# Kernel optimization log

Measured on AMD Instinct MI355X. Metric: run time of the kernel, lower is better.

Reference implementation:

```python
import jax, jax.numpy as jnp
import numpy as np

B, N, C, H = 8, 1024, 512, 8
DH = C // H
SCALE = DH ** -0.5
NEG = -1.0e9


def setup_inputs() -> dict:
    key = jax.random.key(0)
    ks = jax.random.split(key, 8)
    s = lambda fan: 1.0 / np.sqrt(fan)
    return {
        "x": jax.random.normal(ks[0], (B, N, C), jnp.float32),
        "mask": jnp.ones((B, N), jnp.float32),
        "qkv_w": jax.random.normal(ks[1], (3 * C, C), jnp.float32) * s(C),
        "qkv_b": jnp.zeros((3 * C,), jnp.float32),
        "proj_w_mat": jax.random.normal(ks[2], (C, C), jnp.float32) * s(C),
        "proj_b": jnp.zeros((C,), jnp.float32),
        "pl_w": jax.random.normal(ks[3], (H, H), jnp.float32) * s(H),
        "pl_b": jnp.zeros((H,), jnp.float32),
        "pw_w": jax.random.normal(ks[4], (H, H), jnp.float32) * s(H),
        "pw_b": jnp.zeros((H,), jnp.float32),
    }


def reference(x, mask, qkv_w, qkv_b, proj_w_mat, proj_b, pl_w, pl_b, pw_w, pw_b):
    b, n, c = x.shape
    h = pl_w.shape[0]
    dh = c // h
    # qkv: [B,N,3C] -> [3,B,H,N,Dh]
    qkv = (x @ qkv_w.T + qkv_b).reshape(b, n, 3, h, dh).transpose(2, 0, 3, 1, 4)
    q, k, v = qkv[0] * SCALE, qkv[1], qkv[2]
    # raw scores [B,H,N,N]
    attn = jnp.einsum("bhnd,bhmd->bhnm", q, k)
    # talking-heads pre-softmax mixing (Linear over head dim)
    attn = jnp.einsum("bhnm,gh->bgnm", attn, pl_w) + pl_b[None, :, None, None]
    # mask: [B,N] -> broadcast over heads and query dim (keys masked)
    attn = attn + (1.0 - mask)[:, None, None, :] * NEG
    attn = jax.nn.softmax(attn, axis=-1)
    # talking-heads post-softmax mixing
    attn = jnp.einsum("bhnm,gh->bgnm", attn, pw_w) + pw_b[None, :, None, None]
    out = jnp.einsum("bhnm,bhmd->bhnd", attn, v)
    out = out.transpose(0, 2, 1, 3).reshape(b, n, c)
    out = out @ proj_w_mat.T + proj_b
    return (out, attn)
```

## Files before the change

kernel.cpp:

```cpp
#include <hip/hip_runtime.h>
#include <cstddef>

#define B_ 8
#define N_ 1024
#define C_ 512
#define H_ 8
#define DH_ 64
#define QKVLD 1536
#define SCALE_ 0.125f
#define NEG_ -1.0e9f
#define ESHIFT 6.0f

typedef _Float16 f16;
typedef f16  f16x4 __attribute__((ext_vector_type(4)));
typedef f16  f16x8 __attribute__((ext_vector_type(8)));
typedef float f32x4 __attribute__((ext_vector_type(4)));

static __device__ __forceinline__ f16x4 cvt4(float4 v) {
    f16x4 r; r[0] = (f16)v.x; r[1] = (f16)v.y; r[2] = (f16)v.z; r[3] = (f16)v.w;
    return r;
}

__global__ __launch_bounds__(256) void k_qkv(const float* __restrict__ A,
                                             const float* __restrict__ Bt,
                                             const float* __restrict__ bias,
                                             float* __restrict__ Cc) {
    const int lda = C_, ldb = C_, ldc = QKVLD, K = C_;
    const int bm = blockIdx.y * 128, bn = blockIdx.x * 128;
    __shared__ __align__(16) f16 Af[128][40];
    __shared__ __align__(16) f16 Bf[128][40];
    const int tid  = threadIdx.x;
    const int wid  = tid >> 6, lane = tid & 63;
    const int wm   = (wid >> 1) * 64, wn = (wid & 1) * 64;
    const int lrow = lane & 15, kg = lane >> 4;
    const int ar = tid >> 3, ac = (tid & 7) << 2;

    f32x4 acc[4][4];
#pragma unroll
    for (int i = 0; i < 4; ++i)
#pragma unroll
        for (int j = 0; j < 4; ++j) acc[i][j] = (f32x4){0.f, 0.f, 0.f, 0.f};

    for (int k0 = 0; k0 < K; k0 += 32) {
        float4 a0 = *(const float4*)(A  + (size_t)(bm + ar     ) * lda + k0 + ac);
        float4 a1 = *(const float4*)(A  + (size_t)(bm + ar + 32) * lda + k0 + ac);
        float4 a2 = *(const float4*)(A  + (size_t)(bm + ar + 64) * lda + k0 + ac);
        float4 a3 = *(const float4*)(A  + (size_t)(bm + ar + 96) * lda + k0 + ac);
        float4 b0 = *(const float4*)(Bt + (size_t)(bn + ar     ) * ldb + k0 + ac);
        float4 b1 = *(const float4*)(Bt + (size_t)(bn + ar + 32) * ldb + k0 + ac);
        float4 b2 = *(const float4*)(Bt + (size_t)(bn + ar + 64) * ldb + k0 + ac);
        float4 b3 = *(const float4*)(Bt + (size_t)(bn + ar + 96) * ldb + k0 + ac);
        __syncthreads();
        *(f16x4*)&Af[ar     ][ac] = cvt4(a0);
        *(f16x4*)&Af[ar + 32][ac] = cvt4(a1);
        *(f16x4*)&Af[ar + 64][ac] = cvt4(a2);
        *(f16x4*)&Af[ar + 96][ac] = cvt4(a3);
        *(f16x4*)&Bf[ar     ][ac] = cvt4(b0);
        *(f16x4*)&Bf[ar + 32][ac] = cvt4(b1);
        *(f16x4*)&Bf[ar + 64][ac] = cvt4(b2);
        *(f16x4*)&Bf[ar + 96][ac] = cvt4(b3);
        __syncthreads();
        f16x8 af[4], bfv[4];
#pragma unroll
        for (int i = 0; i < 4; ++i)
            af[i] = *(const f16x8*)&Af[wm + i * 16 + lrow][kg * 8];
#pragma unroll
        for (int j = 0; j < 4; ++j)
            bfv[j] = *(const f16x8*)&Bf[wn + j * 16 + lrow][kg * 8];
#pragma unroll
        for (int i = 0; i < 4; ++i)
#pragma unroll
            for (int j = 0; j < 4; ++j)
                acc[i][j] = __builtin_amdgcn_mfma_f32_16x16x32_f16(af[i], bfv[j], acc[i][j], 0, 0, 0);
    }
#pragma unroll
    for (int j = 0; j < 4; ++j) {
        const int col = bn + wn + j * 16 + lrow;
        const float bv = bias[col];
#pragma unroll
        for (int i = 0; i < 4; ++i) {
            const int row0 = bm + wm + i * 16 + kg * 4;
#pragma unroll
            for (int r = 0; r < 4; ++r)
                Cc[(size_t)(row0 + r) * ldc + col] = acc[i][j][r] + bv;
        }
    }
}

__global__ __launch_bounds__(256) void pack_kf(const float* __restrict__ qkv,
                                               f16* __restrict__ kf) {
    const size_t i8 = ((size_t)blockIdx.x * 256 + threadIdx.x) << 3;
    const size_t row = i8 >> 9;
    const int c = (int)(i8 & 511);
    const float* src = qkv + row * QKVLD + C_ + c;
    float4 v0 = *(const float4*)src;
    float4 v1 = *(const float4*)(src + 4);
    f16x8 o;
    o[0]=(f16)v0.x; o[1]=(f16)v0.y; o[2]=(f16)v0.z; o[3]=(f16)v0.w;
    o[4]=(f16)v1.x; o[5]=(f16)v1.y; o[6]=(f16)v1.z; o[7]=(f16)v1.w;
    *(f16x8*)(kf + i8) = o;
}

__global__ __launch_bounds__(256) void pack_pw(const float* __restrict__ w,
                                               f16* __restrict__ wf) {
    const size_t i8 = ((size_t)blockIdx.x * 256 + threadIdx.x) << 3;
    const float* src = w + i8;
    float4 v0 = *(const float4*)src;
    float4 v1 = *(const float4*)(src + 4);
    f16x8 o;
    o[0]=(f16)v0.x; o[1]=(f16)v0.y; o[2]=(f16)v0.z; o[3]=(f16)v0.w;
    o[4]=(f16)v1.x; o[5]=(f16)v1.y; o[6]=(f16)v1.z; o[7]=(f16)v1.w;
    *(f16x8*)(wf + i8) = o;
}

__global__ __launch_bounds__(256) void pack_vt(const float* __restrict__ qkv,
                                               f16* __restrict__ vt) {
    const int z = blockIdx.x, b = z >> 3, h = z & 7;
    const float* V = qkv + (size_t)b * N_ * QKVLD + 2 * C_ + h * DH_;
    f16* O = vt + (size_t)z * DH_ * N_;
    __shared__ __align__(16) f16 T[64][72];
    const int t = threadIdx.x;
    for (int m0 = 0; m0 < N_; m0 += 64) {
#pragma unroll
        for (int it = 0; it < 4; ++it) {
            const int m = (t >> 4) + it * 16, d = (t & 15) * 4;
            float4 v = *(const float4*)(V + (size_t)(m0 + m) * QKVLD + d);
            T[d + 0][m] = (f16)v.x; T[d + 1][m] = (f16)v.y;
            T[d + 2][m] = (f16)v.z; T[d + 3][m] = (f16)v.w;
        }
        __syncthreads();
#pragma unroll
        for (int it = 0; it < 2; ++it) {
            const int d = (t >> 3) + it * 32, m = (t & 7) << 3;
            *(f16x8*)(O + (size_t)d * N_ + m0 + m) = *(const f16x8*)&T[d][m];
        }
        __syncthreads();
    }
}

__global__ __launch_bounds__(512, 3) void k_scorexp(
    const float* __restrict__ qkv,
    const f16*  __restrict__ kf,
    const float* __restrict__ mask,
    const float* __restrict__ pl_w, const float* __restrict__ pl_b,
    f16* __restrict__ p16,
    float* __restrict__ stats)
{
    __shared__ __align__(16) f16 Qs[16][520];
    __shared__ __align__(16) f16 Ps[8][16][136];
    __shared__ float Stat[8][8][16];

    const int flat = blockIdx.x;
    const int b = flat & 7, qt = flat >> 3;
    const int q0 = qt * 16;
    const int tid = threadIdx.x;
    const int w = tid >> 6, l = tid & 63;
    const int lc = l & 15, lr4 = l >> 4;

    {
        const int qrow = tid >> 5, c0 = (tid & 31) << 4;
        const float* src = qkv + (size_t)(b * N_ + q0 + qrow) * QKVLD + c0;
#pragma unroll
        for (int c = 0; c < 16; c += 4) {
            float4 v = *(const float4*)(src + c);
            f16x4 o;
            o[0]=(f16)(v.x*SCALE_); o[1]=(f16)(v.y*SCALE_);
            o[2]=(f16)(v.z*SCALE_); o[3]=(f16)(v.w*SCALE_);
            *(f16x4*)&Qs[qrow][c0 + c] = o;
        }
    }
    __syncthreads();

    const f16* kfb = kf + (size_t)b * N_ * C_;
    const float* maskb = mask + b * N_;

    float sm[8];
#pragma unroll
    for (int g = 0; g < 8; ++g) sm[g] = 0.f;

    for (int mt = 0; mt < N_; mt += 128) {
        const int mb = mt + (w << 4);
        float4 mk4 = *(const float4*)(maskb + mb + (lr4 << 2));
        float mkv[4] = {(1.f-mk4.x)*NEG_, (1.f-mk4.y)*NEG_,
                        (1.f-mk4.z)*NEG_, (1.f-mk4.w)*NEG_};
        float a[8][4];
#pragma unroll
        for (int g = 0; g < 8; ++g) {
            const float bb = pl_b[g];
#pragma unroll
            for (int r = 0; r < 4; ++r) a[g][r] = bb + mkv[r];
        }
        const f16* krow = kfb + (size_t)(mb + lc) * C_ + (lr4 << 3);
        f16x8 kfr[16];
#pragma unroll
        for (int t = 0; t < 16; ++t)
            kfr[t] = *(const f16x8*)(krow + (t << 5));
#pragma unroll
        for (int h = 0; h < 8; ++h) {
            f16x8 qa = *(const f16x8*)&Qs[lc][(h << 6) + (lr4 << 3)];
            f16x8 qb = *(const f16x8*)&Qs[lc][(h << 6) + 32 + (lr4 << 3)];
            f32x4 s = (f32x4){0.f, 0.f, 0.f, 0.f};
            s = __builtin_amdgcn_mfma_f32_16x16x32_f16(kfr[2*h    ], qa, s, 0, 0, 0);
            s = __builtin_amdgcn_mfma_f32_16x16x32_f16(kfr[2*h + 1], qb, s, 0, 0, 0);
#pragma unroll
            for (int g = 0; g < 8; ++g) {
                const float wv = pl_w[(g << 3) + h];
#pragma unroll
                for (int r = 0; r < 4; ++r) a[g][r] = fmaf(wv, s[r], a[g][r]);
            }
        }
#pragma unroll
        for (int g = 0; g < 8; ++g) {
            f16x4 ph;
#pragma unroll
            for (int r = 0; r < 4; ++r) {
                float e = __expf(a[g][r] - ESHIFT);
                sm[g] += e;
                ph[r] = (f16)e;
            }
            *(f16x4*)&Ps[g][lc][(w << 4) + (lr4 << 2)] = ph;
        }
        __syncthreads();
        {
            const int mseg = (l & 15) << 3;
            const int qb0 = l >> 4;
#pragma unroll
            for (int qq = 0; qq < 4; ++qq) {
                const int q = qb0 + (qq << 2);
                f16x8 v = *(const f16x8*)&Ps[w][q][mseg];
                f16* dst = p16 + (((size_t)(b * N_ + q0 + q) << 3) + w) * N_ + mt + mseg;
                __builtin_nontemporal_store(v, (f16x8*)dst);
            }
        }
        __syncthreads();
    }
#pragma unroll
    for (int g = 0; g < 8; ++g) {
        sm[g] += __shfl_xor(sm[g], 16);
        sm[g] += __shfl_xor(sm[g], 32);
    }
    if (l < 16) {
#pragma unroll
        for (int g = 0; g < 8; ++g) Stat[w][g][l] = sm[g];
    }
    __syncthreads();
    if (tid < 16) {
#pragma unroll
        for (int g = 0; g < 8; ++g) {
            float S = 0.f;
#pragma unroll
            for (int wv = 0; wv < 8; ++wv) S += Stat[wv][g][tid];
            stats[((size_t)((b << 3) + g)) * N_ + q0 + tid] = 1.f / S;
        }
    }
}

__global__ __launch_bounds__(512, 4) void k_post(
    const f16*  __restrict__ p16,
    const f16*  __restrict__ vt,
    const f16*  __restrict__ pwf,
    const float* __restrict__ pw_w, const float* __restrict__ pw_b,
    const float* __restrict__ proj_b,
    const float* __restrict__ stats,
    float* __restrict__ attn,
    float* __restrict__ out)
{
    __shared__ __align__(16) f16 Pl[8][16][68];
    __shared__ __align__(16) f16 Ps[8][16][68];
    __shared__ float iS[8][16];

    const int flat = blockIdx.x;
    const int b = flat & 7, qt = flat >> 3;
    const int q0 = qt * 16;
    const int tid = threadIdx.x;
    const int w = tid >> 6, l = tid & 63;
    const int lc = l & 15, lr4 = l >> 4;

    if (tid < 128) {
        const int g = tid >> 4, q = tid & 15;
        iS[g][q] = stats[((size_t)((b << 3) + g)) * N_ + q0 + q];
    }
    float Wg[8];
#pragma unroll
    for (int g = 0; g < 8; ++g) Wg[g] = pw_w[(w << 3) + g];
    const float bw = pw_b[w];

    f32x4 O[4];
#pragma unroll
    for (int df = 0; df < 4; ++df) O[df] = (f32x4){0.f, 0.f, 0.f, 0.f};

    float* attnb = attn + (size_t)(b * H_) * N_ * N_;
    const f16* vg = vt + (size_t)(b * H_ + w) * DH_ * N_;

    const int lrow = tid >> 2;
    const int lg = lrow >> 4, lq = lrow & 15;
    const int lseg = (tid & 3) << 4;
    const f16* lsrc = p16 + (((size_t)(b * N_ + q0 + lq) << 3) + lg) * N_ + lseg;

    for (int mt = 0; mt < N_; mt += 64) {
        __syncthreads();
        {
            f16x8 v0 = *(const f16x8*)(lsrc + mt);
            f16x8 v1 = *(const f16x8*)(lsrc + mt + 8);
            *(f16x8*)&Pl[lg][lq][lseg]     = v0;
            *(f16x8*)&Pl[lg][lq][lseg + 8] = v1;
        }
        __syncthreads();
#pragma unroll
        for (int qq = 0; qq < 4; ++qq) {
            const int q = lr4 + (qq << 2);
            const int mc = lc << 2;
            float p0 = bw, p1 = bw, p2v = bw, p3 = bw;
#pragma unroll
            for (int g = 0; g < 8; ++g) {
                f16x4 pg = *(const f16x4*)&Pl[g][q][mc];
                const float wv = Wg[g] * iS[g][q];
                p0 = fmaf(wv, (float)pg[0], p0);
                p1 = fmaf(wv, (float)pg[1], p1);
                p2v = fmaf(wv, (float)pg[2], p2v);
                p3 = fmaf(wv, (float)pg[3], p3);
            }
            f32x4 r = (f32x4){p0, p1, p2v, p3};
            __builtin_nontemporal_store(r,
                (f32x4*)(attnb + ((size_t)w * N_ + q0 + q) * N_ + mt + mc));
            f16x4 ph; ph[0]=(f16)p0; ph[1]=(f16)p1; ph[2]=(f16)p2v; ph[3]=(f16)p3;
            *(f16x4*)&Ps[w][q][mc] = ph;
        }
#pragma unroll
        for (int kk = 0; kk < 2; ++kk) {
            f16x8 bf = *(const f16x8*)&Ps[w][lc][(kk << 5) + (lr4 << 3)];
#pragma unroll
            for (int df = 0; df < 4; ++df) {
                f16x8 af = *(const f16x8*)(vg + (size_t)((df << 4) + lc) * N_
                                           + mt + (kk << 5) + (lr4 << 3));
                O[df] = __builtin_amdgcn_mfma_f32_16x16x32_f16(af, bf, O[df], 0, 0, 0);
            }
        }
    }

    __syncthreads();
    f16* o1s = (f16*)Ps;
#pragma unroll
    for (int df = 0; df < 4; ++df) {
        f16x4 ph;
        ph[0]=(f16)O[df][0]; ph[1]=(f16)O[df][1];
        ph[2]=(f16)O[df][2]; ph[3]=(f16)O[df][3];
        *(f16x4*)&o1s[lc * 520 + (w << 6) + (df << 4) + (lr4 << 2)] = ph;
    }
    __syncthreads();
    {
        f32x4 acc[4];
#pragma unroll
        for (int cof = 0; cof < 4; ++cof) acc[cof] = (f32x4){0.f, 0.f, 0.f, 0.f};
        for (int ci = 0; ci < C_; ci += 32) {
            f16x8 bf = *(const f16x8*)&o1s[lc * 520 + ci + (lr4 << 3)];
#pragma unroll
            for (int cof = 0; cof < 4; ++cof) {
                f16x8 af = *(const f16x8*)(pwf + (size_t)((w << 6) + (cof << 4) + lc) * C_ + ci + (lr4 << 3));
                acc[cof] = __builtin_amdgcn_mfma_f32_16x16x32_f16(af, bf, acc[cof], 0, 0, 0);
            }
        }
        float* outb = out + (size_t)(b * N_ + q0) * C_;
#pragma unroll
        for (int cof = 0; cof < 4; ++cof) {
            const int co = (w << 6) + (cof << 4) + (lr4 << 2);
            float4 b4 = *(const float4*)(proj_b + co);
            float4 r;
            r.x = acc[cof][0] + b4.x;
            r.y = acc[cof][1] + b4.y;
            r.z = acc[cof][2] + b4.z;
            r.w = acc[cof][3] + b4.w;
            *(float4*)(outb + (size_t)lc * C_ + co) = r;
        }
    }
}

extern "C" void kernel_launch(void* const* d_in, const int* in_sizes, int n_in,
                              void* d_out, int out_size, void* d_ws, size_t ws_size,
                              hipStream_t stream)
{
    const float* x      = (const float*)d_in[0];
    const float* mask   = (const float*)d_in[1];
    const float* qkv_w  = (const float*)d_in[2];
    const float* qkv_b  = (const float*)d_in[3];
    const float* proj_w = (const float*)d_in[4];
    const float* proj_b = (const float*)d_in[5];
    const float* pl_w   = (const float*)d_in[6];
    const float* pl_b   = (const float*)d_in[7];
    const float* pw_w   = (const float*)d_in[8];
    const float* pw_b   = (const float*)d_in[9];

    float* out  = (float*)d_out;
    float* attn = out + (size_t)B_ * N_ * C_;
    float* qkvb = (float*)d_ws;
    f16*   kf   = (f16*)(qkvb + (size_t)B_ * N_ * 3 * C_);
    f16*   vt   = kf + (size_t)B_ * N_ * C_;
    f16*   pwf  = vt + (size_t)B_ * N_ * C_;
    float* stats = (float*)(pwf + (size_t)C_ * C_);
    f16*   p16  = (f16*)(stats + (size_t)B_ * H_ * N_);
    (void)in_sizes; (void)n_in; (void)out_size; (void)ws_size;

    k_qkv<<<dim3(QKVLD / 128, B_ * N_ / 128), 256, 0, stream>>>(x, qkv_w, qkv_b, qkvb);

    pack_kf<<<dim3(2048), 256, 0, stream>>>(qkvb, kf);
    pack_vt<<<dim3(B_ * H_), 256, 0, stream>>>(qkvb, vt);
    pack_pw<<<dim3(128), 256, 0, stream>>>(proj_w, pwf);

    k_scorexp<<<dim3(512), 512, 0, stream>>>(qkvb, kf, mask, pl_w, pl_b, p16, stats);

    k_post<<<dim3(512), 512, 0, stream>>>(
        p16, vt, pwf, pw_w, pw_b, proj_b, stats, attn, out);
}
```

Baseline: 277.7 us.

## Compute post-softmax head mixing directly in MFMA fragment layout, dropping LDS staging

The post-softmax talking-heads mix in k_post is now computed per lane in the exact layout the PV MFMA B-operand needs. Each lane loads all 8 heads' fp16 probabilities straight from global memory, mixes them in registers and feeds the result directly to the MFMA. This removes the per-tile LDS staging buffers, the two __syncthreads per key tile, and the LDS round trip for the mixed probabilities. In exchange, each wave reloads the p16 data for all heads from global or cache (about 8x redundant reads across the 8 waves). The attn stores also change from 16-byte chunks per lane to two 16-byte stores of 8 contiguous floats, giving a different coalescing pattern.

```diff
diff --git a/kernel.cpp b/kernel.cpp
--- a/kernel.cpp
+++ b/kernel.cpp
@@ -265,8 +265,7 @@
     float* __restrict__ attn,
     float* __restrict__ out)
 {
-    __shared__ __align__(16) f16 Pl[8][16][68];
-    __shared__ __align__(16) f16 Ps[8][16][68];
+    __shared__ __align__(16) f16 o1s[16][520];
     __shared__ float iS[8][16];
 
     const int flat = blockIdx.x;
@@ -280,72 +279,58 @@
         const int g = tid >> 4, q = tid & 15;
         iS[g][q] = stats[((size_t)((b << 3) + g)) * N_ + q0 + q];
     }
-    float Wg[8];
-#pragma unroll
-    for (int g = 0; g < 8; ++g) Wg[g] = pw_w[(w << 3) + g];
+    __syncthreads();
+
+    float Wp[8];
+#pragma unroll
+    for (int g = 0; g < 8; ++g) Wp[g] = pw_w[(w << 3) + g] * iS[g][lc];
     const float bw = pw_b[w];
 
     f32x4 O[4];
 #pragma unroll
     for (int df = 0; df < 4; ++df) O[df] = (f32x4){0.f, 0.f, 0.f, 0.f};
 
-    float* attnb = attn + (size_t)(b * H_) * N_ * N_;
     const f16* vg = vt + (size_t)(b * H_ + w) * DH_ * N_;
-
-    const int lrow = tid >> 2;
-    const int lg = lrow >> 4, lq = lrow & 15;
-    const int lseg = (tid & 3) << 4;
-    const f16* lsrc = p16 + (((size_t)(b * N_ + q0 + lq) << 3) + lg) * N_ + lseg;
+    float* arow = attn + ((size_t)(b * H_ + w) * N_ + q0 + lc) * N_;
+    const f16* prow = p16 + ((size_t)(b * N_ + q0 + lc) << 3) * N_;
 
     for (int mt = 0; mt < N_; mt += 64) {
-        __syncthreads();
-        {
-            f16x8 v0 = *(const f16x8*)(lsrc + mt);
-            f16x8 v1 = *(const f16x8*)(lsrc + mt + 8);
-            *(f16x8*)&Pl[lg][lq][lseg]     = v0;
-            *(f16x8*)&Pl[lg][lq][lseg + 8] = v1;
-        }
-        __syncthreads();
-#pragma unroll
-        for (int qq = 0; qq < 4; ++qq) {
-            const int q = lr4 + (qq << 2);
-            const int mc = lc << 2;
-            float p0 = bw, p1 = bw, p2v = bw, p3 = bw;
-#pragma unroll
-            for (int g = 0; g < 8; ++g) {
-                f16x4 pg = *(const f16x4*)&Pl[g][q][mc];
-                const float wv = Wg[g] * iS[g][q];
-                p0 = fmaf(wv, (float)pg[0], p0);
-                p1 = fmaf(wv, (float)pg[1], p1);
-                p2v = fmaf(wv, (float)pg[2], p2v);
-                p3 = fmaf(wv, (float)pg[3], p3);
-            }
-            f32x4 r = (f32x4){p0, p1, p2v, p3};
-            __builtin_nontemporal_store(r,
-                (f32x4*)(attnb + ((size_t)w * N_ + q0 + q) * N_ + mt + mc));
-            f16x4 ph; ph[0]=(f16)p0; ph[1]=(f16)p1; ph[2]=(f16)p2v; ph[3]=(f16)p3;
-            *(f16x4*)&Ps[w][q][mc] = ph;
-        }
 #pragma unroll
         for (int kk = 0; kk < 2; ++kk) {
-            f16x8 bf = *(const f16x8*)&Ps[w][lc][(kk << 5) + (lr4 << 3)];
+            const int m0 = mt + (kk << 5) + (lr4 << 3);
+            f16x8 pg[8];
+#pragma unroll
+            for (int g = 0; g < 8; ++g)
+                pg[g] = *(const f16x8*)(prow + (size_t)g * N_ + m0);
+            float o[8];
+#pragma unroll
+            for (int j = 0; j < 8; ++j) o[j] = bw;
+#pragma unroll
+            for (int g = 0; g < 8; ++g)
+#pragma unroll
+                for (int j = 0; j < 8; ++j)
+                    o[j] = fmaf(Wp[g], (float)pg[g][j], o[j]);
+            f32x4 lo = (f32x4){o[0], o[1], o[2], o[3]};
+            f32x4 hi = (f32x4){o[4], o[5], o[6], o[7]};
+            __builtin_nontemporal_store(lo, (f32x4*)(arow + m0));
+            __builtin_nontemporal_store(hi, (f32x4*)(arow + m0 + 4));
+            f16x8 bf;
+#pragma unroll
+            for (int j = 0; j < 8; ++j) bf[j] = (f16)o[j];
 #pragma unroll
             for (int df = 0; df < 4; ++df) {
-                f16x8 af = *(const f16x8*)(vg + (size_t)((df << 4) + lc) * N_
-                                           + mt + (kk << 5) + (lr4 << 3));
+                f16x8 af = *(const f16x8*)(vg + (size_t)((df << 4) + lc) * N_ + m0);
                 O[df] = __builtin_amdgcn_mfma_f32_16x16x32_f16(af, bf, O[df], 0, 0, 0);
             }
         }
     }
 
-    __syncthreads();
-    f16* o1s = (f16*)Ps;
 #pragma unroll
     for (int df = 0; df < 4; ++df) {
         f16x4 ph;
         ph[0]=(f16)O[df][0]; ph[1]=(f16)O[df][1];
         ph[2]=(f16)O[df][2]; ph[3]=(f16)O[df][3];
-        *(f16x4*)&o1s[lc * 520 + (w << 6) + (df << 4) + (lr4 << 2)] = ph;
+        *(f16x4*)&o1s[lc][(w << 6) + (df << 4) + (lr4 << 2)] = ph;
     }
     __syncthreads();
     {
@@ -353,7 +338,7 @@
 #pragma unroll
         for (int cof = 0; cof < 4; ++cof) acc[cof] = (f32x4){0.f, 0.f, 0.f, 0.f};
         for (int ci = 0; ci < C_; ci += 32) {
-            f16x8 bf = *(const f16x8*)&o1s[lc * 520 + ci + (lr4 << 3)];
+            f16x8 bf = *(const f16x8*)&o1s[lc][ci + (lr4 << 3)];
 #pragma unroll
             for (int cof = 0; cof < 4; ++cof) {
                 f16x8 af = *(const f16x8*)(pwf + (size_t)((w << 6) + (cof << 4) + lc) * C_ + ci + (lr4 << 3));
```

Measured after the change: 371.2 us. 1.34x slower.

## Split post-softmax kernel over key halves and move output projection to separate kernel

Applied to the files above, without the earlier changes.

k_post now runs on a 2D grid where each block handles half of the key dimension. It writes partial attention-times-V sums to a workspace buffer that reuses the qkv region. A new k_proj kernel adds the two partials and applies the output projection with bias. This doubles the number of blocks for the memory-heavy attention write and raises the occupancy hint. In exchange it adds an extra launch and a round trip of fp32 partials through memory. The attention store also changes from nontemporal to a regular store.

```diff
diff --git a/kernel.cpp b/kernel.cpp
--- a/kernel.cpp
+++ b/kernel.cpp
@@ -255,23 +255,23 @@
     }
 }
 
-__global__ __launch_bounds__(512, 4) void k_post(
+__global__ __launch_bounds__(512, 8) void k_post(
     const f16*  __restrict__ p16,
     const f16*  __restrict__ vt,
-    const f16*  __restrict__ pwf,
     const float* __restrict__ pw_w, const float* __restrict__ pw_b,
-    const float* __restrict__ proj_b,
     const float* __restrict__ stats,
     float* __restrict__ attn,
-    float* __restrict__ out)
+    float* __restrict__ part)
 {
     __shared__ __align__(16) f16 Pl[8][16][68];
     __shared__ __align__(16) f16 Ps[8][16][68];
     __shared__ float iS[8][16];
 
     const int flat = blockIdx.x;
+    const int mh = blockIdx.y;
     const int b = flat & 7, qt = flat >> 3;
     const int q0 = qt * 16;
+    const int mbase = mh << 9;
     const int tid = threadIdx.x;
     const int w = tid >> 6, l = tid & 63;
     const int lc = l & 15, lr4 = l >> 4;
@@ -297,13 +297,13 @@
     const int lseg = (tid & 3) << 4;
     const f16* lsrc = p16 + (((size_t)(b * N_ + q0 + lq) << 3) + lg) * N_ + lseg;
 
-    for (int mt = 0; mt < N_; mt += 64) {
+    for (int mt = mbase; mt < mbase + 512; mt += 64) {
         __syncthreads();
         {
-            f16x8 v0 = *(const f16x8*)(lsrc + mt);
-            f16x8 v1 = *(const f16x8*)(lsrc + mt + 8);
-            *(f16x8*)&Pl[lg][lq][lseg]     = v0;
-            *(f16x8*)&Pl[lg][lq][lseg + 8] = v1;
+            f16x8 c0 = *(const f16x8*)(lsrc + mt);
+            f16x8 c1 = *(const f16x8*)(lsrc + mt + 8);
+            *(f16x8*)&Pl[lg][lq][lseg]     = c0;
+            *(f16x8*)&Pl[lg][lq][lseg + 8] = c1;
         }
         __syncthreads();
 #pragma unroll
@@ -320,9 +320,8 @@
                 p2v = fmaf(wv, (float)pg[2], p2v);
                 p3 = fmaf(wv, (float)pg[3], p3);
             }
-            f32x4 r = (f32x4){p0, p1, p2v, p3};
-            __builtin_nontemporal_store(r,
-                (f32x4*)(attnb + ((size_t)w * N_ + q0 + q) * N_ + mt + mc));
+            *(f32x4*)(attnb + ((size_t)w * N_ + q0 + q) * N_ + mt + mc) =
+                (f32x4){p0, p1, p2v, p3};
             f16x4 ph; ph[0]=(f16)p0; ph[1]=(f16)p1; ph[2]=(f16)p2v; ph[3]=(f16)p3;
             *(f16x4*)&Ps[w][q][mc] = ph;
         }
@@ -338,40 +337,60 @@
         }
     }
 
+    float* pp = part + ((size_t)((mh * B_ + b) * N_) + q0 + lc) * C_ + (w << 6);
+#pragma unroll
+    for (int df = 0; df < 4; ++df)
+        *(f32x4*)(pp + (df << 4) + (lr4 << 2)) = O[df];
+}
+
+__global__ __launch_bounds__(512, 4) void k_proj(
+    const float* __restrict__ part,
+    const f16*  __restrict__ pwf,
+    const float* __restrict__ proj_b,
+    float* __restrict__ out)
+{
+    __shared__ __align__(16) f16 o1s[16][520];
+
+    const int flat = blockIdx.x;
+    const int b = flat & 7, qt = flat >> 3;
+    const int q0 = qt * 16;
+    const int tid = threadIdx.x;
+    const int w = tid >> 6, l = tid & 63;
+    const int lc = l & 15, lr4 = l >> 4;
+
+    const float* p0 = part + ((size_t)(b * N_ + q0 + lc)) * C_ + (w << 6);
+    const float* p1 = part + ((size_t)((B_ + b) * N_ + q0 + lc)) * C_ + (w << 6);
+#pragma unroll
+    for (int df = 0; df < 4; ++df) {
+        const int off = (df << 4) + (lr4 << 2);
+        f32x4 s = *(const f32x4*)(p0 + off) + *(const f32x4*)(p1 + off);
+        f16x4 ph; ph[0]=(f16)s[0]; ph[1]=(f16)s[1]; ph[2]=(f16)s[2]; ph[3]=(f16)s[3];
+        *(f16x4*)&o1s[lc][(w << 6) + off] = ph;
+    }
     __syncthreads();
-    f16* o1s = (f16*)Ps;
-#pragma unroll
-    for (int df = 0; df < 4; ++df) {
-        f16x4 ph;
-        ph[0]=(f16)O[df][0]; ph[1]=(f16)O[df][1];
-        ph[2]=(f16)O[df][2]; ph[3]=(f16)O[df][3];
-        *(f16x4*)&o1s[lc * 520 + (w << 6) + (df << 4) + (lr4 << 2)] = ph;
-    }
-    __syncthreads();
-    {
-        f32x4 acc[4];
-#pragma unroll
-        for (int cof = 0; cof < 4; ++cof) acc[cof] = (f32x4){0.f, 0.f, 0.f, 0.f};
-        for (int ci = 0; ci < C_; ci += 32) {
-            f16x8 bf = *(const f16x8*)&o1s[lc * 520 + ci + (lr4 << 3)];
-#pragma unroll
-            for (int cof = 0; cof < 4; ++cof) {
-                f16x8 af = *(const f16x8*)(pwf + (size_t)((w << 6) + (cof << 4) + lc) * C_ + ci + (lr4 << 3));
-                acc[cof] = __builtin_amdgcn_mfma_f32_16x16x32_f16(af, bf, acc[cof], 0, 0, 0);
-            }
-        }
-        float* outb = out + (size_t)(b * N_ + q0) * C_;
+
+    f32x4 acc[4];
+#pragma unroll
+    for (int cof = 0; cof < 4; ++cof) acc[cof] = (f32x4){0.f, 0.f, 0.f, 0.f};
+    for (int ci = 0; ci < C_; ci += 32) {
+        f16x8 bf = *(const f16x8*)&o1s[lc][ci + (lr4 << 3)];
 #pragma unroll
         for (int cof = 0; cof < 4; ++cof) {
-            const int co = (w << 6) + (cof << 4) + (lr4 << 2);
-            float4 b4 = *(const float4*)(proj_b + co);
-            float4 r;
-            r.x = acc[cof][0] + b4.x;
-            r.y = acc[cof][1] + b4.y;
-            r.z = acc[cof][2] + b4.z;
-            r.w = acc[cof][3] + b4.w;
-            *(float4*)(outb + (size_t)lc * C_ + co) = r;
-        }
+            f16x8 af = *(const f16x8*)(pwf + (size_t)((w << 6) + (cof << 4) + lc) * C_ + ci + (lr4 << 3));
+            acc[cof] = __builtin_amdgcn_mfma_f32_16x16x32_f16(af, bf, acc[cof], 0, 0, 0);
+        }
+    }
+    float* outb = out + (size_t)(b * N_ + q0) * C_;
+#pragma unroll
+    for (int cof = 0; cof < 4; ++cof) {
+        const int co = (w << 6) + (cof << 4) + (lr4 << 2);
+        float4 b4 = *(const float4*)(proj_b + co);
+        float4 r;
+        r.x = acc[cof][0] + b4.x;
+        r.y = acc[cof][1] + b4.y;
+        r.z = acc[cof][2] + b4.z;
+        r.w = acc[cof][3] + b4.w;
+        *(float4*)(outb + (size_t)lc * C_ + co) = r;
     }
 }
 
@@ -398,6 +417,7 @@
     f16*   pwf  = vt + (size_t)B_ * N_ * C_;
     float* stats = (float*)(pwf + (size_t)C_ * C_);
     f16*   p16  = (f16*)(stats + (size_t)B_ * H_ * N_);
+    float* part = qkvb;
     (void)in_sizes; (void)n_in; (void)out_size; (void)ws_size;
 
     k_qkv<<<dim3(QKVLD / 128, B_ * N_ / 128), 256, 0, stream>>>(x, qkv_w, qkv_b, qkvb);
@@ -408,6 +428,8 @@
 
     k_scorexp<<<dim3(512), 512, 0, stream>>>(qkvb, kf, mask, pl_w, pl_b, p16, stats);
 
-    k_post<<<dim3(512), 512, 0, stream>>>(
-        p16, vt, pwf, pw_w, pw_b, proj_b, stats, attn, out);
-}
+    k_post<<<dim3(512, 2), 512, 0, stream>>>(
+        p16, vt, pw_w, pw_b, stats, attn, part);
+
+    k_proj<<<dim3(512), 512, 0, stream>>>(part, pwf, proj_b, out);
+}
```

New measurement: 514.2 us. +85.2%, slower.
